# Kernel optimization log

Measured on AMD Instinct MI355X. Metric: run time of the kernel, lower is better.

## Reference

```python
import jax, jax.numpy as jnp
import numpy as np
from jax import lax

H = 128
N = 4096


def gru_cell(x, h, Wih, Whh, bih, bhh):
    # PyTorch GRU gate order: r, z, n
    gi = x @ Wih + bih
    gh = h @ Whh + bhh
    ir, iz, inn = jnp.split(gi, 3, axis=-1)
    hr, hz, hn = jnp.split(gh, 3, axis=-1)
    r = jax.nn.sigmoid(ir + hr)
    z = jax.nn.sigmoid(iz + hz)
    n = jnp.tanh(inn + r * hn)
    return (1.0 - z) * n + z * h


def setup_inputs() -> dict:
    key = jax.random.key(0)
    ks = jax.random.split(key, 32)
    s = 0.02
    rn = lambda k, shp, sc=s: (jax.random.normal(k, shp, jnp.float32) * sc)
    inp = {
        'boxes_feature': jax.random.normal(ks[0], (1, N, 1024), jnp.float32),
        'boxes_box_score': jax.random.normal(ks[1], (1, N, 2560), jnp.float32),
        'boxes_box': jax.random.normal(ks[2], (1, N, 320), jnp.float32),
        'boxes_label': jax.random.uniform(ks[3], (1, N), jnp.float32),
        'boxes_weight': jax.random.uniform(ks[4], (1, N), jnp.float32),
        'boxes_num': N,
        'W_appear': rn(ks[5], (1024, H)), 'b_appear': jnp.zeros((H,), jnp.float32),
        'W_s1': rn(ks[6], (2560, 512)), 'b_s1': jnp.zeros((512,), jnp.float32),
        'W_s2': rn(ks[7], (512, H)), 'b_s2': jnp.zeros((H,), jnp.float32),
        'W_box': rn(ks[8], (320, H)), 'b_box': jnp.zeros((H,), jnp.float32),
        'W_all': rn(ks[9], (3 * H, H)), 'b_all': jnp.zeros((H,), jnp.float32),
        'enc_Wih': rn(ks[10], (H, 3 * H)), 'enc_Whh': rn(ks[11], (H, 3 * H)),
        'enc_bih': jnp.zeros((3 * H,), jnp.float32), 'enc_bhh': jnp.zeros((3 * H,), jnp.float32),
        'dec_Wih': rn(ks[12], (H, 3 * H)), 'dec_Whh': rn(ks[13], (H, 3 * H)),
        'dec_bih': jnp.zeros((3 * H,), jnp.float32), 'dec_bhh': jnp.zeros((3 * H,), jnp.float32),
        'W_attn': rn(ks[14], (2 * H, 1)), 'b_attn': jnp.zeros((1,), jnp.float32),
        'W_comb': rn(ks[15], (2 * H, H)), 'b_comb': jnp.zeros((H,), jnp.float32),
        'W_out': rn(ks[16], (H, 1)), 'b_out': jnp.zeros((1,), jnp.float32),
    }
    return inp


def reference(boxes_feature, boxes_box_score, boxes_box, boxes_label, boxes_weight, boxes_num,
              W_appear, b_appear, W_s1, b_s1, W_s2, b_s2, W_box, b_box, W_all, b_all,
              enc_Wih, enc_Whh, enc_bih, enc_bhh, dec_Wih, dec_Whh, dec_bih, dec_bhh,
              W_attn, b_attn, W_comb, b_comb, W_out, b_out):
    n = boxes_num
    h = W_appear.shape[1]
    # per-proposal feature fusion
    ef = jax.nn.relu(boxes_feature[0, :n] @ W_appear + b_appear)            # [N, h]
    es = jax.nn.relu((boxes_box_score[0, :n] @ W_s1 + b_s1) @ W_s2 + b_s2)  # [N, h]
    eb = jax.nn.relu(boxes_box[0, :n] @ W_box + b_box)                       # [N, h]
    X = jax.nn.relu(jnp.concatenate([ef, es, eb], axis=1) @ W_all + b_all)   # [N, h]

    # encoder GRU over proposals (batch=1)
    def enc_step(hc, x):
        hn = gru_cell(x, hc, enc_Wih, enc_Whh, enc_bih, enc_bhh)
        return hn, hn
    h0 = jnp.zeros((h,), X.dtype)
    h_enc, E = lax.scan(enc_step, h0, X)  # E: [N, h]

    # Bahdanau-style attention; NOTE: original softmaxes each [1,1] score over
    # dim=1, so every weight is exactly 1.0. We keep softmax for faithful grads.
    Xw = X @ W_attn[h:]  # [N, 1], constant part of the attn score

    def dec_step(hc, x):
        scores = hc @ W_attn[:h] + b_attn + Xw          # [N, 1]
        w = jax.nn.softmax(scores, axis=1)              # [N, 1] == all ones
        applied = w[:, 0] @ E                           # [h]
        din = jax.nn.relu(jnp.concatenate([x, applied]) @ W_comb + b_comb)
        hn = gru_cell(din, hc, dec_Wih, dec_Whh, dec_bih, dec_bhh)
        return hn, hn

    _, D = lax.scan(dec_step, h_enc, X)  # D: [N, h]
    output = jax.nn.sigmoid(D @ W_out + b_out)  # [N, 1]
    return output, boxes_label[0, :n], boxes_weight[0, :n]
```

## Files before the change

kernel.cpp:

```cpp
#include <hip/hip_runtime.h>
#include <hip/hip_bf16.h>
#include <math.h>

#define NBOX 4096
#define HDIM 128
#define G3   384
#define PF   8

typedef _Float16 half2v __attribute__((ext_vector_type(2)));
typedef short bf16x8 __attribute__((ext_vector_type(8)));
typedef float f32x4 __attribute__((ext_vector_type(4)));
#define LDK 40

__device__ __forceinline__ float sigm(float x) { return 1.f / (1.f + expf(-x)); }
__device__ __forceinline__ float sigm_fast(float x) {
    return __builtin_amdgcn_rcpf(1.f + __expf(-x));
}
__device__ __forceinline__ float tanh_fast(float x) {
    x = fminf(15.f, fmaxf(-15.f, x));
    const float e2 = __expf(2.f * x);
    return (e2 - 1.f) * __builtin_amdgcn_rcpf(e2 + 1.f);
}
__device__ __forceinline__ float bcast_q1(float x) {
    return __int_as_float(__builtin_amdgcn_mov_dpp(__float_as_int(x), 0x55, 0xF, 0xF, false));
}
__device__ __forceinline__ float bcast_q3(float x) {
    return __int_as_float(__builtin_amdgcn_mov_dpp(__float_as_int(x), 0xFF, 0xF, 0xF, false));
}
__device__ __forceinline__ float qsum(float v) {
    asm("v_add_f32_dpp %0, %0, %0 quad_perm:[1,0,3,2] row_mask:0xf bank_mask:0xf"
        : "+v"(v));
    asm("v_add_f32_dpp %0, %0, %0 quad_perm:[2,3,0,1] row_mask:0xf bank_mask:0xf"
        : "+v"(v));
    return v;
}
__device__ __forceinline__ float fdot2(unsigned int h2, unsigned int w2, float acc) {
    return __builtin_amdgcn_fdot2(__builtin_bit_cast(half2v, h2),
                                  __builtin_bit_cast(half2v, w2), acc, false);
}
__device__ __forceinline__ void bar_lds() {
    asm volatile("s_waitcnt lgkmcnt(0)\n\ts_barrier" ::: "memory");
}
__device__ __forceinline__ unsigned short f2bf(float x) {
    return __builtin_bit_cast(unsigned short, __float2bfloat16(x));
}

struct ConvArgs {
    const float* B[8];
    unsigned short* Bt[8];
    int K[8], N[8];
    int blk0[9];
};
__global__ __launch_bounds__(256) void conv_all(ConvArgs a)
{
    const int bid = blockIdx.x;
    int s = 0;
    while (s < 7 && bid >= a.blk0[s + 1]) ++s;
    const int id = (bid - a.blk0[s]) * 256 + threadIdx.x;
    const int K = a.K[s], N = a.N[s];
    if (id < K * N) {
        const int n = id / K, k = id % K;
        a.Bt[s][(size_t)n * K + k] = f2bf(a.B[s][(size_t)k * N + n]);
    }
}

__global__ __launch_bounds__(256) void gemm_bf16t(
    const float* __restrict__ A, const unsigned short* __restrict__ Bt,
    const float* __restrict__ bias, float* __restrict__ C,
    int M, int N, int K, int ldc, int act)
{
    __shared__ unsigned short As[128][LDK];
    __shared__ unsigned short Bs[128][LDK];
    const int tid = threadIdx.x;
    const int m0 = blockIdx.y * 128, n0 = blockIdx.x * 128;
    const int wv = tid >> 6, lane = tid & 63;
    const int wr = (wv >> 1) * 64, wc = (wv & 1) * 64;
    const int lr = lane & 15, lk = lane >> 4;
    const int sm = tid >> 1, skh = (tid & 1) * 16;
    f32x4 acc[4][4] = {};
    for (int k0 = 0; k0 < K; k0 += 32) {
        const float* ga = &A[(size_t)(m0 + sm) * K + k0 + skh];
        float4 f0 = *(const float4*)(ga + 0);
        float4 f1 = *(const float4*)(ga + 4);
        float4 f2 = *(const float4*)(ga + 8);
        float4 f3 = *(const float4*)(ga + 12);
        const float fa[16] = {f0.x,f0.y,f0.z,f0.w, f1.x,f1.y,f1.z,f1.w,
                              f2.x,f2.y,f2.z,f2.w, f3.x,f3.y,f3.z,f3.w};
        unsigned int pk[8];
#pragma unroll
        for (int e = 0; e < 8; ++e)
            pk[e] = (unsigned int)f2bf(fa[2*e]) | ((unsigned int)f2bf(fa[2*e+1]) << 16);
        *(uint4*)&As[sm][skh]     = make_uint4(pk[0], pk[1], pk[2], pk[3]);
        *(uint4*)&As[sm][skh + 8] = make_uint4(pk[4], pk[5], pk[6], pk[7]);
        const uint4* gb = (const uint4*)&Bt[(size_t)(n0 + sm) * K + k0 + skh];
        *(uint4*)&Bs[sm][skh]     = gb[0];
        *(uint4*)&Bs[sm][skh + 8] = gb[1];
        __syncthreads();
        bf16x8 af[4], bfr[4];
#pragma unroll
        for (int f = 0; f < 4; ++f) {
            af[f]  = *(const bf16x8*)&As[wr + f * 16 + lr][lk * 8];
            bfr[f] = *(const bf16x8*)&Bs[wc + f * 16 + lr][lk * 8];
        }
#pragma unroll
        for (int i = 0; i < 4; ++i)
#pragma unroll
            for (int j = 0; j < 4; ++j)
                acc[i][j] = __builtin_amdgcn_mfma_f32_16x16x32_bf16(
                    af[i], bfr[j], acc[i][j], 0, 0, 0);
        __syncthreads();
    }
#pragma unroll
    for (int i = 0; i < 4; ++i)
#pragma unroll
        for (int j = 0; j < 4; ++j)
#pragma unroll
            for (int r = 0; r < 4; ++r) {
                const int row = m0 + wr + i * 16 + lk * 4 + r;
                const int col = n0 + wc + j * 16 + lr;
                float v = acc[i][j][r] + bias[col];
                if (act) v = fmaxf(v, 0.f);
                C[(size_t)row * ldc + col] = v;
            }
}

__global__ __launch_bounds__(256)
__attribute__((amdgpu_waves_per_eu(1, 1)))
void gru_scan(
    const float* __restrict__ GI, const float* __restrict__ Whh,
    const float* __restrict__ bhh, const float* __restrict__ h0,
    double* __restrict__ esum_out, float* __restrict__ hfinal_out,
    float* __restrict__ D_out, int T)
{
    __shared__ unsigned short h16[2][HDIM];
    const int tid = threadIdx.x;
    const int j = tid >> 2;
    const int g = tid & 3;
    const int qa = 2 * j, qb = 2 * j + 1;
    const int myq = (g & 2) ? qb : qa;
    const int colS = ((g & 1) ? HDIM : 0) + myq;
    const int colT = 2 * HDIM + myq;
    unsigned int w[96];
#pragma unroll
    for (int c6 = 0; c6 < 6; ++c6) {
        const int cc = (c6 % 3) * HDIM + ((c6 < 3) ? qa : qb);
#pragma unroll
        for (int p2 = 0; p2 < 16; ++p2) {
            const int k = 32 * g + 2 * p2;
            const _Float16 lo = (_Float16)Whh[(size_t)k * G3 + cc];
            const _Float16 hi = (_Float16)Whh[(size_t)(k + 1) * G3 + cc];
            w[c6 * 16 + p2] = (unsigned int)__builtin_bit_cast(unsigned short, lo)
                            | ((unsigned int)__builtin_bit_cast(unsigned short, hi) << 16);
        }
    }
#pragma unroll
    for (int p = 0; p < 96; ++p) asm volatile("" : "+v"(w[p]));
    const float bS = bhh[colS];
    const float bT = bhh[colT];
    if (tid < HDIM)
        h16[0][tid] = __builtin_bit_cast(unsigned short,
                                         (_Float16)(h0 ? h0[tid] : 0.f));
    float hp = (float)(_Float16)(h0 ? h0[myq] : 0.f);
    double esum = 0.0;
    float gS[PF], gT[PF], gSn[PF], gTn[PF];
#pragma unroll
    for (int p = 0; p < PF; ++p) {
        gS[p] = GI[(size_t)p * G3 + colS];
        gT[p] = GI[(size_t)p * G3 + colT];
    }
    __syncthreads();
    for (int t0 = 0; t0 < T; t0 += PF) {
#pragma unroll
        for (int p = 0; p < PF; ++p) {
            gSn[p] = GI[(size_t)(t0 + PF + p) * G3 + colS];
            gTn[p] = GI[(size_t)(t0 + PF + p) * G3 + colT];
        }
#pragma unroll
        for (int p = 0; p < PF; ++p) {
            const int t = t0 + p;
            const uint4* hb = (const uint4*)h16[t & 1];
            uint4 uu[4];
#pragma unroll
            for (int pp = 0; pp < 4; ++pp) uu[pp] = hb[4 * g + pp];
            float s0 = 0.f, s1 = 0.f, s2 = 0.f, s3 = 0.f, s4 = 0.f, s5 = 0.f;
#pragma unroll
            for (int pp = 0; pp < 4; ++pp) {
                const unsigned int x[4] = {uu[pp].x, uu[pp].y, uu[pp].z, uu[pp].w};
#pragma unroll
                for (int i2 = 0; i2 < 4; ++i2) {
                    const int pi = 4 * pp + i2;
                    s0 = fdot2(x[i2], w[pi], s0);
                    s1 = fdot2(x[i2], w[16 + pi], s1);
                    s2 = fdot2(x[i2], w[32 + pi], s2);
                    s3 = fdot2(x[i2], w[48 + pi], s3);
                    s4 = fdot2(x[i2], w[64 + pi], s4);
                    s5 = fdot2(x[i2], w[80 + pi], s5);
                }
            }
            s0 = qsum(s0); s1 = qsum(s1); s2 = qsum(s2);
            s3 = qsum(s3); s4 = qsum(s4); s5 = qsum(s5);
            const float ghS = ((g & 2) ? ((g & 1) ? s4 : s3)
                                       : ((g & 1) ? s1 : s0)) + bS;
            const float ghT = ((g & 2) ? s5 : s2) + bT;
            const float s = sigm_fast(gS[p] + ghS);
            const float n = tanh_fast(gT[p] + s * ghT);
            const float z1 = bcast_q1(s);
            const float z3 = bcast_q3(s);
            const float z = (g & 2) ? z3 : z1;
            const float hn = z * (hp - n) + n;
            if (!(g & 1)) {
                h16[(t + 1) & 1][myq] =
                    __builtin_bit_cast(unsigned short, (_Float16)hn);
                esum += (double)hn;
                if (D_out) D_out[(size_t)t * HDIM + myq] = hn;
            }
            hp = (float)(_Float16)hn;
            bar_lds();
        }
#pragma unroll
        for (int p = 0; p < PF; ++p) { gS[p] = gSn[p]; gT[p] = gTn[p]; }
    }
    if (!(g & 1)) {
        if (esum_out) esum_out[myq] = esum;
        if (hfinal_out) hfinal_out[myq] = hp;
    }
}

__global__ void prep_dec(const double* __restrict__ esum, const float* __restrict__ W_comb,
                         const float* __restrict__ b_comb, float* __restrict__ c2)
{
    __shared__ double es[HDIM];
    const int j = threadIdx.x;
    es[j] = esum[j];
    __syncthreads();
    double acc = (double)b_comb[j];
    for (int k = 0; k < HDIM; ++k)
        acc += es[k] * (double)W_comb[(HDIM + k) * HDIM + j];
    c2[j] = (float)acc;
}

__global__ __launch_bounds__(256) void epilogue(
    const float* __restrict__ D, const float* __restrict__ Wout,
    const float* __restrict__ b_out, const float* __restrict__ lab,
    const float* __restrict__ wt, float* __restrict__ out)
{
    const int bid = blockIdx.x;
    if (bid < 1024) {
        const int row = (bid * 256 + threadIdx.x) >> 6;
        const int lane = threadIdx.x & 63;
        float v = D[(size_t)row * HDIM + lane] * Wout[lane]
                + D[(size_t)row * HDIM + 64 + lane] * Wout[64 + lane];
#pragma unroll
        for (int s = 32; s > 0; s >>= 1) v += __shfl_down(v, s);
        if (lane == 0) out[row] = sigm(v + b_out[0]);
    } else {
        const int i = (bid - 1024) * 256 + threadIdx.x;
        out[NBOX + i] = (i < NBOX) ? lab[i] : wt[i - NBOX];
    }
}

extern "C" void kernel_launch(void* const* d_in, const int* in_sizes, int n_in,
                              void* d_out, int out_size, void* d_ws, size_t ws_size,
                              hipStream_t stream)
{
    const float* boxes_feature = (const float*)d_in[0];
    const float* boxes_score   = (const float*)d_in[1];
    const float* boxes_box     = (const float*)d_in[2];
    const float* boxes_label   = (const float*)d_in[3];
    const float* boxes_weight  = (const float*)d_in[4];
    const float* W_appear = (const float*)d_in[6];
    const float* b_appear = (const float*)d_in[7];
    const float* W_s1     = (const float*)d_in[8];
    const float* b_s1     = (const float*)d_in[9];
    const float* W_s2     = (const float*)d_in[10];
    const float* b_s2     = (const float*)d_in[11];
    const float* W_box    = (const float*)d_in[12];
    const float* b_box    = (const float*)d_in[13];
    const float* W_all    = (const float*)d_in[14];
    const float* b_all    = (const float*)d_in[15];
    const float* enc_Wih  = (const float*)d_in[16];
    const float* enc_Whh  = (const float*)d_in[17];
    const float* enc_bih  = (const float*)d_in[18];
    const float* enc_bhh  = (const float*)d_in[19];
    const float* dec_Wih  = (const float*)d_in[20];
    const float* dec_Whh  = (const float*)d_in[21];
    const float* dec_bih  = (const float*)d_in[22];
    const float* dec_bhh  = (const float*)d_in[23];
    const float* W_comb   = (const float*)d_in[26];
    const float* b_comb   = (const float*)d_in[27];
    const float* W_out    = (const float*)d_in[28];
    const float* b_out    = (const float*)d_in[29];

    float* out = (float*)d_out;
    float* ws = (float*)d_ws;
    size_t o = 0;
    float* T1   = ws + o; o += (size_t)NBOX * 512;
    float* XCAT = ws + o; o += (size_t)NBOX * G3;
    float* X    = ws + o; o += (size_t)NBOX * HDIM;
    float* GIE  = ws + o; o += (size_t)(NBOX + PF) * G3;
    float* GID  = ws + o; o += (size_t)(NBOX + PF) * G3;
    float* DIN  = ws + o; o += (size_t)NBOX * HDIM;
    float* D    = ws + o; o += (size_t)NBOX * HDIM;
    o = (o + 1) & ~(size_t)1;
    double* esum = (double*)(ws + o); o += 256;
    float* henc = ws + o; o += 128;
    float* c2   = ws + o; o += 128;

    unsigned short* ws1t   = (unsigned short*)GIE;
    unsigned short* wappt  = ws1t + 1310720;
    unsigned short* ws2t   = wappt + 131072;
    unsigned short* wboxt  = ws2t + 65536;
    unsigned short* wallt  = wboxt + 40960;
    unsigned short* encwt  = (unsigned short*)GID;
    unsigned short* wcombt = encwt + 49152;
    unsigned short* decwt  = (unsigned short*)D;

    ConvArgs ca;
    ca.B[0]=W_s1;    ca.Bt[0]=ws1t;   ca.K[0]=2560; ca.N[0]=512;
    ca.B[1]=W_appear;ca.Bt[1]=wappt;  ca.K[1]=1024; ca.N[1]=128;
    ca.B[2]=W_s2;    ca.Bt[2]=ws2t;   ca.K[2]=512;  ca.N[2]=128;
    ca.B[3]=W_box;   ca.Bt[3]=wboxt;  ca.K[3]=320;  ca.N[3]=128;
    ca.B[4]=W_all;   ca.Bt[4]=wallt;  ca.K[4]=384;  ca.N[4]=128;
    ca.B[5]=enc_Wih; ca.Bt[5]=encwt;  ca.K[5]=128;  ca.N[5]=384;
    ca.B[6]=W_comb;  ca.Bt[6]=wcombt; ca.K[6]=128;  ca.N[6]=128;
    ca.B[7]=dec_Wih; ca.Bt[7]=decwt;  ca.K[7]=128;  ca.N[7]=384;
    {
        int acc_blk = 0;
        for (int s = 0; s < 8; ++s) {
            ca.blk0[s] = acc_blk;
            acc_blk += (ca.K[s] * ca.N[s] + 255) / 256;
        }
        ca.blk0[8] = acc_blk;
        conv_all<<<acc_blk, 256, 0, stream>>>(ca);
    }

    gemm_bf16t<<<dim3(4, 32), 256, 0, stream>>>(
        boxes_score, ws1t, b_s1, T1, NBOX, 512, 2560, 512, 0);
    gemm_bf16t<<<dim3(1, 32), 256, 0, stream>>>(
        boxes_feature, wappt, b_appear, XCAT + 0, NBOX, 128, 1024, G3, 1);
    gemm_bf16t<<<dim3(1, 32), 256, 0, stream>>>(
        T1, ws2t, b_s2, XCAT + HDIM, NBOX, 128, 512, G3, 1);
    gemm_bf16t<<<dim3(1, 32), 256, 0, stream>>>(
        boxes_box, wboxt, b_box, XCAT + 2 * HDIM, NBOX, 128, 320, G3, 1);
    gemm_bf16t<<<dim3(1, 32), 256, 0, stream>>>(
        XCAT, wallt, b_all, X, NBOX, 128, 384, HDIM, 1);

    gemm_bf16t<<<dim3(3, 32), 256, 0, stream>>>(
        X, encwt, enc_bih, GIE, NBOX, 384, 128, G3, 0);
    gru_scan<<<1, 256, 0, stream>>>(GIE, enc_Whh, enc_bhh, nullptr,
                                    esum, henc, nullptr, NBOX);

    prep_dec<<<1, 128, 0, stream>>>(esum, W_comb, b_comb, c2);
    gemm_bf16t<<<dim3(1, 32), 256, 0, stream>>>(
        X, wcombt, c2, DIN, NBOX, 128, 128, HDIM, 1);
    gemm_bf16t<<<dim3(3, 32), 256, 0, stream>>>(
        DIN, decwt, dec_bih, GID, NBOX, 384, 128, G3, 0);

    gru_scan<<<1, 256, 0, stream>>>(GID, dec_Whh, dec_bhh, henc,
                                    nullptr, nullptr, D, NBOX);

    epilogue<<<1024 + 32, 256, 0, stream>>>(D, W_out, b_out,
                                            boxes_label, boxes_weight, out);
}
```

Measured before the change: 3.359 ms.

## Fold W_s1 and W_s2 into one weight matrix, simplify tanh, drop fp16 hp rounding

The score branch applies W_s1 (2560x512) and then W_s2 (512x128) with no activation between them, so the code precomputes W_s1@W_s2 and a fused bias once per call. It then runs a single 2560->128 GEMM on the box scores instead of a 512-wide GEMM followed by a second GEMM. This cuts the GEMM work over the 4096 boxes by roughly 4x for that branch, at the cost of a small weight-fusion GEMM plus extra conversion kernels. It also shortens tanh_fast by removing the clamp and rewriting it as 1-2/(e^2x+1), and keeps the previous hidden state in fp32 instead of rounding it to fp16. Both change numerics slightly.

```diff
diff --git a/kernel.cpp b/kernel.cpp
--- a/kernel.cpp
+++ b/kernel.cpp
@@ -17,9 +17,8 @@
     return __builtin_amdgcn_rcpf(1.f + __expf(-x));
 }
 __device__ __forceinline__ float tanh_fast(float x) {
-    x = fminf(15.f, fmaxf(-15.f, x));
     const float e2 = __expf(2.f * x);
-    return (e2 - 1.f) * __builtin_amdgcn_rcpf(e2 + 1.f);
+    return 1.f - 2.f * __builtin_amdgcn_rcpf(e2 + 1.f);
 }
 __device__ __forceinline__ float bcast_q1(float x) {
     return __int_as_float(__builtin_amdgcn_mov_dpp(__float_as_int(x), 0x55, 0xF, 0xF, false));
@@ -46,22 +45,44 @@
 }
 
 struct ConvArgs {
-    const float* B[8];
-    unsigned short* Bt[8];
-    int K[8], N[8];
-    int blk0[9];
+    const float* B[7];
+    unsigned short* Bt[7];
+    int K[7], N[7];
+    int blk0[8];
 };
 __global__ __launch_bounds__(256) void conv_all(ConvArgs a)
 {
     const int bid = blockIdx.x;
     int s = 0;
-    while (s < 7 && bid >= a.blk0[s + 1]) ++s;
+    while (s < 6 && bid >= a.blk0[s + 1]) ++s;
     const int id = (bid - a.blk0[s]) * 256 + threadIdx.x;
     const int K = a.K[s], N = a.N[s];
     if (id < K * N) {
         const int n = id / K, k = id % K;
         a.Bt[s][(size_t)n * K + k] = f2bf(a.B[s][(size_t)k * N + n]);
     }
+}
+
+__global__ __launch_bounds__(256) void conv_bt(
+    const float* __restrict__ B, unsigned short* __restrict__ Bt, int K, int N)
+{
+    const int id = blockIdx.x * 256 + threadIdx.x;
+    if (id < K * N) {
+        const int n = id / K, k = id % K;
+        Bt[(size_t)n * K + k] = f2bf(B[(size_t)k * N + n]);
+    }
+}
+
+__global__ void bias_fuse(const float* __restrict__ b_s1, const float* __restrict__ W_s2,
+                          const float* __restrict__ b_s2, float* __restrict__ bfused,
+                          float* __restrict__ zero128)
+{
+    const int j = threadIdx.x;
+    double acc = (double)b_s2[j];
+    for (int c = 0; c < 512; ++c)
+        acc += (double)b_s1[c] * (double)W_s2[c * HDIM + j];
+    bfused[j] = (float)acc;
+    zero128[j] = 0.f;
 }
 
 __global__ __launch_bounds__(256) void gemm_bf16t(
@@ -160,7 +181,7 @@
     if (tid < HDIM)
         h16[0][tid] = __builtin_bit_cast(unsigned short,
                                          (_Float16)(h0 ? h0[tid] : 0.f));
-    float hp = (float)(_Float16)(h0 ? h0[myq] : 0.f);
+    float hp = h0 ? h0[myq] : 0.f;
     double esum = 0.0;
     float gS[PF], gT[PF], gSn[PF], gTn[PF];
 #pragma unroll
@@ -214,7 +235,7 @@
                 esum += (double)hn;
                 if (D_out) D_out[(size_t)t * HDIM + myq] = hn;
             }
-            hp = (float)(_Float16)hn;
+            hp = hn;
             bar_lds();
         }
 #pragma unroll
@@ -306,8 +327,11 @@
     float* henc = ws + o; o += 128;
     float* c2   = ws + o; o += 128;
 
-    unsigned short* ws1t   = (unsigned short*)GIE;
-    unsigned short* wappt  = ws1t + 1310720;
+    float* wf32          = T1;
+    unsigned short* wfut = (unsigned short*)(T1 + 327680);
+    float* zero128       = T1 + 491520;
+    float* bfused        = T1 + 491648;
+    unsigned short* wappt  = (unsigned short*)GIE;
     unsigned short* ws2t   = wappt + 131072;
     unsigned short* wboxt  = ws2t + 65536;
     unsigned short* wallt  = wboxt + 40960;
@@ -316,30 +340,32 @@
     unsigned short* decwt  = (unsigned short*)D;
 
     ConvArgs ca;
-    ca.B[0]=W_s1;    ca.Bt[0]=ws1t;   ca.K[0]=2560; ca.N[0]=512;
-    ca.B[1]=W_appear;ca.Bt[1]=wappt;  ca.K[1]=1024; ca.N[1]=128;
-    ca.B[2]=W_s2;    ca.Bt[2]=ws2t;   ca.K[2]=512;  ca.N[2]=128;
-    ca.B[3]=W_box;   ca.Bt[3]=wboxt;  ca.K[3]=320;  ca.N[3]=128;
-    ca.B[4]=W_all;   ca.Bt[4]=wallt;  ca.K[4]=384;  ca.N[4]=128;
-    ca.B[5]=enc_Wih; ca.Bt[5]=encwt;  ca.K[5]=128;  ca.N[5]=384;
-    ca.B[6]=W_comb;  ca.Bt[6]=wcombt; ca.K[6]=128;  ca.N[6]=128;
-    ca.B[7]=dec_Wih; ca.Bt[7]=decwt;  ca.K[7]=128;  ca.N[7]=384;
+    ca.B[0]=W_appear; ca.Bt[0]=wappt;  ca.K[0]=1024; ca.N[0]=128;
+    ca.B[1]=W_s2;     ca.Bt[1]=ws2t;   ca.K[1]=512;  ca.N[1]=128;
+    ca.B[2]=W_box;    ca.Bt[2]=wboxt;  ca.K[2]=320;  ca.N[2]=128;
+    ca.B[3]=W_all;    ca.Bt[3]=wallt;  ca.K[3]=384;  ca.N[3]=128;
+    ca.B[4]=enc_Wih;  ca.Bt[4]=encwt;  ca.K[4]=128;  ca.N[4]=384;
+    ca.B[5]=W_comb;   ca.Bt[5]=wcombt; ca.K[5]=128;  ca.N[5]=128;
+    ca.B[6]=dec_Wih;  ca.Bt[6]=decwt;  ca.K[6]=128;  ca.N[6]=384;
     {
         int acc_blk = 0;
-        for (int s = 0; s < 8; ++s) {
+        for (int s = 0; s < 7; ++s) {
             ca.blk0[s] = acc_blk;
             acc_blk += (ca.K[s] * ca.N[s] + 255) / 256;
         }
-        ca.blk0[8] = acc_blk;
+        ca.blk0[7] = acc_blk;
         conv_all<<<acc_blk, 256, 0, stream>>>(ca);
     }
-
-    gemm_bf16t<<<dim3(4, 32), 256, 0, stream>>>(
-        boxes_score, ws1t, b_s1, T1, NBOX, 512, 2560, 512, 0);
+    bias_fuse<<<1, 128, 0, stream>>>(b_s1, W_s2, b_s2, bfused, zero128);
+
+    gemm_bf16t<<<dim3(1, 2560 / 128), 256, 0, stream>>>(
+        W_s1, ws2t, zero128, wf32, 2560, 128, 512, 128, 0);
+    conv_bt<<<(2560 * 128 + 255) / 256, 256, 0, stream>>>(wf32, wfut, 2560, 128);
+
+    gemm_bf16t<<<dim3(1, 32), 256, 0, stream>>>(
+        boxes_score, wfut, bfused, XCAT + HDIM, NBOX, 128, 2560, G3, 1);
     gemm_bf16t<<<dim3(1, 32), 256, 0, stream>>>(
         boxes_feature, wappt, b_appear, XCAT + 0, NBOX, 128, 1024, G3, 1);
-    gemm_bf16t<<<dim3(1, 32), 256, 0, stream>>>(
-        T1, ws2t, b_s2, XCAT + HDIM, NBOX, 128, 512, G3, 1);
     gemm_bf16t<<<dim3(1, 32), 256, 0, stream>>>(
         boxes_box, wboxt, b_box, XCAT + 2 * HDIM, NBOX, 128, 320, G3, 1);
     gemm_bf16t<<<dim3(1, 32), 256, 0, stream>>>(
```

Result: no change. 3.357 ms (-0.0%).
